# Kernel optimization log

Hardware: AMD Instinct MI355X
Metric: run time of the kernel (lower is better)

## Reference

```python
import jax, jax.numpy as jnp
import numpy as np

N, DIM, HEADS, E = 20000, 256, 4, 100000
C = DIM  # TransformerConv out_channels per head (concat=False averages heads)


def setup_inputs() -> dict:
    key = jax.random.key(0)
    ks = jax.random.split(key, 12)
    s = DIM ** -0.5
    w = lambda k, shape: jax.random.normal(k, shape, jnp.float32) * s
    z = lambda shape: jnp.zeros(shape, jnp.float32)
    return {
        "f_all": jax.random.normal(ks[0], (N, DIM), jnp.float32),
        "edge_index": jax.random.randint(ks[1], (2, E), 0, N),
        "W_gcn": w(ks[2], (DIM, DIM)), "b_gcn": z((DIM,)),
        "W_q": w(ks[3], (DIM, HEADS * C)), "b_q": z((HEADS * C,)),
        "W_k": w(ks[4], (DIM, HEADS * C)), "b_k": z((HEADS * C,)),
        "W_v": w(ks[5], (DIM, HEADS * C)), "b_v": z((HEADS * C,)),
        "W_skip": w(ks[6], (DIM, DIM)), "b_skip": z((DIM,)),
        "W_beta": w(ks[7], (3 * DIM, 1)),
        "W_cnn": w(ks[8], (DIM, DIM)), "b_cnn": z((DIM,)),
    }


def reference(f_all, edge_index, W_gcn, b_gcn, W_q, b_q, W_k, b_k, W_v, b_v,
              W_skip, b_skip, W_beta, W_cnn, b_cnn):
    src, dst = edge_index[0], edge_index[1]

    # --- GCNConv: add self loops, symmetric D^-1/2 (A+I) D^-1/2 normalization ---
    loop = jnp.arange(N)
    s2 = jnp.concatenate([src, loop])
    d2 = jnp.concatenate([dst, loop])
    deg = jax.ops.segment_sum(jnp.ones_like(d2, jnp.float32), d2, N)
    dinv = jnp.where(deg > 0, 1.0 / jnp.sqrt(deg), 0.0)
    norm = dinv[s2] * dinv[d2]                    # [E+N]
    h = f_all @ W_gcn                             # [N, DIM]
    x = jax.ops.segment_sum(h[s2] * norm[:, None], d2, N) + b_gcn
    x = jax.nn.relu(x)

    # --- TransformerConv(heads=H, concat=False, beta=True) ---
    q = (x @ W_q + b_q).reshape(N, HEADS, C)
    k = (x @ W_k + b_k).reshape(N, HEADS, C)
    v = (x @ W_v + b_v).reshape(N, HEADS, C)
    logits = jnp.einsum('ehc,ehc->eh', q[dst], k[src]) / np.float32(np.sqrt(C))
    m = jax.ops.segment_max(logits, dst, N)       # per-target max for stable softmax
    e = jnp.exp(logits - m[dst])
    denom = jax.ops.segment_sum(e, dst, N)
    alpha = e / jnp.maximum(denom[dst], 1e-16)    # [E, H]
    agg = jax.ops.segment_sum(v[src] * alpha[:, :, None], dst, N)  # [N, H, C]
    out = agg.mean(axis=1)                        # concat=False -> head average
    xr = x @ W_skip + b_skip                      # root/skip branch
    beta = jax.nn.sigmoid(jnp.concatenate([out, xr, out - xr], axis=-1) @ W_beta)
    tf = jax.nn.relu(beta * xr + (1.0 - beta) * out)  # [N, DIM]

    # --- Conv1d with kernel (dim,1) on [1,1,dim,N]: per-node linear, output [dim,N] ---
    conv = jnp.einsum('cd,nd->cn', W_cnn, tf) + b_cnn[:, None]  # [DIM, N]
    # torch does .view(1, n_mole, -1) on the [1,dim,1,N] conv output: raw reshape
    return conv.reshape(1, N, DIM)
```

## Files before the change

kernel.cpp:

```cpp
#include <hip/hip_runtime.h>
#include <math.h>

#define DIMC 256
#define NHEAD 4
#define CAP 64

typedef unsigned short bf16u;
typedef __attribute__((ext_vector_type(8))) short bf16x8;
typedef __attribute__((ext_vector_type(4))) float f32x4;

typedef __attribute__((address_space(1))) const unsigned char ga_u8;
typedef __attribute__((address_space(3))) unsigned char lds_u8;
__device__ __forceinline__ void gld_lds16(const void* g, void* l) {
    __builtin_amdgcn_global_load_lds((ga_u8*)g, (lds_u8*)l, 16, 0, 0);
}

__device__ __forceinline__ bf16u f2bf(float f) {
    union { float f; unsigned int i; } c; c.f = f;
    unsigned int r = c.i + 0x7fffu + ((c.i >> 16) & 1u);
    return (bf16u)(r >> 16);
}
__device__ __forceinline__ void store_bf4(bf16u* p, float4 v) {
    ushort4 raw;
    raw.x = f2bf(v.x); raw.y = f2bf(v.y); raw.z = f2bf(v.z); raw.w = f2bf(v.w);
    *(ushort4*)p = raw;
}
__device__ __forceinline__ void load_bf8(const bf16u* p, float* o) {
    bf16x8 raw = *(const bf16x8*)p;
#pragma unroll
    for (int i = 0; i < 8; ++i) {
        union { float f; unsigned int u; } c;
        c.u = ((unsigned int)(unsigned short)raw[i]) << 16;
        o[i] = c.f;
    }
}
__device__ __forceinline__ void store_bf8(bf16u* p, const float* v) {
    bf16x8 raw;
#pragma unroll
    for (int i = 0; i < 8; ++i) raw[i] = (short)f2bf(v[i]);
    *(bf16x8*)p = raw;
}


__global__ void fill_kernel(const int* __restrict__ src, const int* __restrict__ dst,
                            int* __restrict__ cursor, int* __restrict__ srcs, int E) {
    int e = blockIdx.x * 256 + threadIdx.x;
    if (e < E) {
        int d = dst[e];
        int pos = atomicAdd(&cursor[d], 1);
        if (pos < CAP) srcs[d * CAP + pos] = src[e];
    }
}


__global__ __launch_bounds__(256) void prep_kernel(
    const float* __restrict__ f_all, int n4_f,
    const float* __restrict__ W_gcn, const float* __restrict__ W_q,
    const float* __restrict__ W_k, const float* __restrict__ W_v,
    const float* __restrict__ W_skip, const float* __restrict__ W_cnn,
    const float* __restrict__ b_q, const float* __restrict__ b_v,
    const float* __restrict__ b_skip,
    bf16u* __restrict__ xbuf, bf16u* __restrict__ WgcnT,
    bf16u* __restrict__ BTyp, bf16u* __restrict__ BT_vs,
    bf16u* __restrict__ Wcnn_b,
    float* __restrict__ ybias, float* __restrict__ bvm,
    int* __restrict__ cursor, int N) {
    __shared__ __align__(16) char sh[40960];
    int b = blockIdx.x, t = threadIdx.x;
    int nf = (n4_f + 255) >> 8;
    int nz = (N + 255) >> 8;

    if (b < 16) {
        bf16u (*As)[128][32] = (bf16u(*)[128][32])sh;
        bf16u (*Bs)[128][32] = (bf16u(*)[128][32])(sh + 16384);
        bf16u (*Cs)[128]     = (bf16u(*)[128])(sh + 32768);
        int rb = b >> 1, cb = b & 1;
        int h = rb >> 1;
        int j0 = (rb & 1) * 128;
        int t0 = h * 256;
        int w = t >> 6, lane = t & 63;
        int q = lane >> 4, r = lane & 15;
        int wm = (w & 1) * 64, wn = (w >> 1) * 64;
        int srow = t >> 2, scol = (t & 3) * 8;
        const float* ak0 = W_k + (size_t)(j0 + srow) * 1024 + t0 + scol;
        const float* ak1 = W_k + (size_t)(j0 + 64 + srow) * 1024 + t0 + scol;
        const float* bq0 = W_q + (size_t)(cb * 128 + srow) * 1024 + t0 + scol;
        const float* bq1 = W_q + (size_t)(cb * 128 + 64 + srow) * 1024 + t0 + scol;
        auto stage = [&](const float* gp, bf16u* lp) {
            float4 u = *(const float4*)gp, v = *(const float4*)(gp + 4);
            bf16x8 o;
            o[0] = (short)f2bf(u.x); o[1] = (short)f2bf(u.y);
            o[2] = (short)f2bf(u.z); o[3] = (short)f2bf(u.w);
            o[4] = (short)f2bf(v.x); o[5] = (short)f2bf(v.y);
            o[6] = (short)f2bf(v.z); o[7] = (short)f2bf(v.w);
            *(bf16x8*)lp = o;
        };
        f32x4 acc[4][4] = {};
        for (int g = 0; g < 4; ++g) {
            int k0 = g * 64;
            stage(ak0 + k0,      &As[0][srow][scol]);
            stage(ak1 + k0,      &As[0][64 + srow][scol]);
            stage(ak0 + k0 + 32, &As[1][srow][scol]);
            stage(ak1 + k0 + 32, &As[1][64 + srow][scol]);
            stage(bq0 + k0,      &Bs[0][srow][scol]);
            stage(bq1 + k0,      &Bs[0][64 + srow][scol]);
            stage(bq0 + k0 + 32, &Bs[1][srow][scol]);
            stage(bq1 + k0 + 32, &Bs[1][64 + srow][scol]);
            __syncthreads();
#pragma unroll
            for (int ks = 0; ks < 2; ++ks) {
                bf16x8 af[4], bfr[4];
#pragma unroll
                for (int i = 0; i < 4; ++i) af[i] = *(const bf16x8*)&As[ks][wm + i * 16 + r][q * 8];
#pragma unroll
                for (int j = 0; j < 4; ++j) bfr[j] = *(const bf16x8*)&Bs[ks][wn + j * 16 + r][q * 8];
#pragma unroll
                for (int i = 0; i < 4; ++i)
#pragma unroll
                    for (int j = 0; j < 4; ++j)
                        acc[i][j] = __builtin_amdgcn_mfma_f32_16x16x32_bf16(af[i], bfr[j], acc[i][j], 0, 0, 0);
            }
            __syncthreads();
        }
        int bm = rb * 128, bn = cb * 128;
        int rhalf = (w & 1) * 16;
        int colbase = (w >> 1) * 64;
#pragma unroll
        for (int i = 0; i < 4; ++i) {
#pragma unroll
            for (int j = 0; j < 4; ++j)
#pragma unroll
                for (int rg = 0; rg < 4; ++rg)
                    Cs[rhalf + q * 4 + rg][colbase + j * 16 + r] = f2bf(acc[i][j][rg] * 0.0625f);
            __syncthreads();
#pragma unroll
            for (int cpass = 0; cpass < 2; ++cpass) {
                int chunk = cpass * 256 + t;
                int sr = chunk >> 4;
                int c16 = chunk & 15;
                int grow = bm + (sr < 16 ? i * 16 + sr : 64 + i * 16 + (sr - 16));
                *(bf16x8*)&BTyp[(size_t)grow * 256 + bn + c16 * 8] = *(const bf16x8*)&Cs[sr][c16 * 8];
            }
            __syncthreads();
        }
        return;
    }
    b -= 16;
    if (b < nf) {
        int i = b * 256 + t;
        if (i < n4_f) {
            float4 vv = *(const float4*)(f_all + (size_t)i * 4);
            store_bf4(xbuf + (size_t)i * 4, vv);
        }
        return;
    }
    b -= nf;
    if (b < 64) {
        int i = b * 256 + t;
        float4 vv = *(const float4*)(W_cnn + (size_t)i * 4);
        store_bf4(Wcnn_b + (size_t)i * 4, vv);
        return;
    }
    b -= 64;
    if (b < 4) {
        int h = b, j = t;
        const float4* bq4 = (const float4*)(b_q + h * 256);
        const float4* wk4 = (const float4*)(W_k + (size_t)j * 1024 + h * 256);
        float acc = 0.f;
        for (int u = 0; u < 64; ++u) {
            float4 a = bq4[u], w = wk4[u];
            acc += a.x * w.x + a.y * w.y + a.z * w.z + a.w * w.w;
        }
        ybias[h * 256 + j] = acc * 0.0625f;
        return;
    }
    b -= 4;
    if (b < 1) {
        ybias[1024 + t] = b_skip[t];
        bvm[t] = 0.25f * (b_v[t] + b_v[256 + t] + b_v[512 + t] + b_v[768 + t]);
        return;
    }
    b -= 1;
    if (b < nz) {
        int i = b * 256 + t;
        if (i < N) cursor[i] = 0;
        return;
    }
    b -= nz;
    float (*T)[33] = (float(*)[33])sh;
    const float* src; bf16u* dst;
    int inld, inrow0, incol0, outld, outrow0, outcol0;
    if (b < 64) {
        int N0 = (b & 7) * 32, K0 = (b >> 3) * 32;
        src = W_gcn; inld = 256; inrow0 = K0; incol0 = N0;
        dst = WgcnT; outld = 256; outrow0 = N0; outcol0 = K0;
    } else if (b < 128) {
        int bb = b - 64; int N0 = (bb & 7) * 32, K0 = (bb >> 3) * 32;
        src = W_skip; inld = 256; inrow0 = K0; incol0 = N0;
        dst = BTyp;  outld = 256; outrow0 = 1024 + N0; outcol0 = K0;
    } else {
        int bb = b - 128; int jt = bb & 7, ct = (bb >> 3) & 7, hh = bb >> 6;
        src = W_v;  inld = 1024; inrow0 = ct * 32; incol0 = hh * 256 + jt * 32;
        dst = BT_vs; outld = 1024; outrow0 = jt * 32; outcol0 = hh * 256 + ct * 32;
    }
    int tx = t & 31, ty = t >> 5;
#pragma unroll
    for (int i = 0; i < 4; ++i)
        T[ty + 8 * i][tx] = src[(size_t)(inrow0 + ty + 8 * i) * inld + incol0 + tx];
    __syncthreads();
#pragma unroll
    for (int i = 0; i < 4; ++i)
        dst[(size_t)(outrow0 + ty + 8 * i) * outld + outcol0 + tx] = f2bf(T[tx][ty + 8 * i]);
}


template <bool ROWBIAS>
__global__ __launch_bounds__(256) void gemm_tile(const bf16u* __restrict__ A,
                                                 const bf16u* __restrict__ BT,
                                                 const float* __restrict__ bias,
                                                 void* __restrict__ Cout,
                                                 int M, int Nc, int ldc, int K) {
    __shared__ __align__(16) bf16u As[2][128][32];
    __shared__ __align__(16) bf16u Bs[2][128][32];
    int t = threadIdx.x;
    int w = t >> 6, lane = t & 63;
    int q = lane >> 4, r = lane & 15;
    int wm = (w & 1) * 64, wn = (w >> 1) * 64;
    int bm = blockIdx.y * 128, bn = blockIdx.x * 128;

    int srow = t >> 2, scol = (t & 3) * 8;
    int arow0 = bm + srow;      if (arow0 >= M)  arow0 = M - 1;
    int arow1 = bm + 64 + srow; if (arow1 >= M)  arow1 = M - 1;
    int brow0 = bn + srow;      if (brow0 >= Nc) brow0 = Nc - 1;
    int brow1 = bn + 64 + srow; if (brow1 >= Nc) brow1 = Nc - 1;
    const bf16u* a0 = A + (size_t)arow0 * K + scol;
    const bf16u* a1 = A + (size_t)arow1 * K + scol;
    const bf16u* b0 = BT + (size_t)brow0 * K + scol;
    const bf16u* b1 = BT + (size_t)brow1 * K + scol;

    char* As_base = (char*)&As[0][0][0] + w * 1024;
    char* Bs_base = (char*)&Bs[0][0][0] + w * 1024;

    f32x4 acc[4][4] = {};
    int ngroups = K >> 6;
    for (int g = 0; g < ngroups; ++g) {
        int k0 = g * 64;
        gld_lds16(a0 + k0, As_base);
        gld_lds16(a1 + k0, As_base + 4096);
        gld_lds16(b0 + k0, Bs_base);
        gld_lds16(b1 + k0, Bs_base + 4096);
        gld_lds16(a0 + k0 + 32, As_base + 8192);
        gld_lds16(a1 + k0 + 32, As_base + 8192 + 4096);
        gld_lds16(b0 + k0 + 32, Bs_base + 8192);
        gld_lds16(b1 + k0 + 32, Bs_base + 8192 + 4096);
        __syncthreads();
#pragma unroll
        for (int ks = 0; ks < 2; ++ks) {
            bf16x8 af[4], bfr[4];
#pragma unroll
            for (int i = 0; i < 4; ++i) af[i] = *(const bf16x8*)&As[ks][wm + i * 16 + r][q * 8];
#pragma unroll
            for (int j = 0; j < 4; ++j) bfr[j] = *(const bf16x8*)&Bs[ks][wn + j * 16 + r][q * 8];
#pragma unroll
            for (int i = 0; i < 4; ++i)
#pragma unroll
                for (int j = 0; j < 4; ++j)
                    acc[i][j] = __builtin_amdgcn_mfma_f32_16x16x32_bf16(af[i], bfr[j], acc[i][j], 0, 0, 0);
        }
        __syncthreads();
    }

    if (ROWBIAS) {
        float* C = (float*)Cout;
#pragma unroll
        for (int j = 0; j < 4; ++j) {
            int col = bn + wn + j * 16 + r;
            if (col >= Nc) continue;
#pragma unroll
            for (int i = 0; i < 4; ++i)
#pragma unroll
                for (int rg = 0; rg < 4; ++rg) {
                    int row = bm + wm + i * 16 + q * 4 + rg;
                    if (row < M)
                        __builtin_nontemporal_store(acc[i][j][rg] + bias[row],
                                                    &C[(size_t)row * ldc + col]);
                }
        }
    } else {
        __shared__ __align__(16) bf16u Cs[32][128];
        bf16u* C = (bf16u*)Cout;
        float cb4[4];
#pragma unroll
        for (int j = 0; j < 4; ++j) {
            int col = bn + wn + j * 16 + r;
            cb4[j] = bias ? bias[col] : 0.0f;
        }
        int rhalf = (w & 1) * 16;
        int colbase = (w >> 1) * 64;
        __syncthreads();
#pragma unroll
        for (int i = 0; i < 4; ++i) {
#pragma unroll
            for (int j = 0; j < 4; ++j)
#pragma unroll
                for (int rg = 0; rg < 4; ++rg)
                    Cs[rhalf + q * 4 + rg][colbase + j * 16 + r] = f2bf(acc[i][j][rg] + cb4[j]);
            __syncthreads();
#pragma unroll
            for (int cpass = 0; cpass < 2; ++cpass) {
                int chunk = cpass * 256 + t;
                int sr = chunk >> 4;
                int c16 = chunk & 15;
                int grow = bm + (sr < 16 ? i * 16 + sr : 64 + i * 16 + (sr - 16));
                if (grow < M)
                    __builtin_nontemporal_store(*(const bf16x8*)&Cs[sr][c16 * 8],
                                                (bf16x8*)&C[(size_t)grow * ldc + bn + c16 * 8]);
            }
            __syncthreads();
        }
    }
}


__global__ __launch_bounds__(256) void gcn_agg_kernel(const bf16u* __restrict__ h,
                                                      const int* __restrict__ cursor,
                                                      const int* __restrict__ srcs,
                                                      const float* __restrict__ b_gcn,
                                                      bf16u* __restrict__ x, int N) {
    int n = blockIdx.x * 8 + (threadIdx.x >> 5);
    if (n >= N) return;
    int lane = threadIdx.x & 31;
    int cb = lane * 8;
    int cnt = cursor[n]; if (cnt > CAP) cnt = CAP;
    float dn = rsqrtf((float)(cnt + 1));
    float hn[8];
    load_bf8(h + (size_t)n * DIMC + cb, hn);
    int base = n * CAP;
    float acc[8] = {};
    int i = 0;
    for (; i + 4 <= cnt; i += 4) {
        int4 s4 = *(const int4*)(srcs + base + i);
        float d0 = rsqrtf((float)(cursor[s4.x] + 1));
        float d1 = rsqrtf((float)(cursor[s4.y] + 1));
        float d2 = rsqrtf((float)(cursor[s4.z] + 1));
        float d3 = rsqrtf((float)(cursor[s4.w] + 1));
        float h0[8], h1[8], h2[8], h3[8];
        load_bf8(h + (size_t)s4.x * DIMC + cb, h0);
        load_bf8(h + (size_t)s4.y * DIMC + cb, h1);
        load_bf8(h + (size_t)s4.z * DIMC + cb, h2);
        load_bf8(h + (size_t)s4.w * DIMC + cb, h3);
#pragma unroll
        for (int j = 0; j < 8; ++j)
            acc[j] += h0[j] * d0 + h1[j] * d1 + h2[j] * d2 + h3[j] * d3;
    }
    for (; i < cnt; ++i) {
        int s = srcs[base + i];
        float ds = rsqrtf((float)(cursor[s] + 1));
        float hv[8];
        load_bf8(h + (size_t)s * DIMC + cb, hv);
#pragma unroll
        for (int j = 0; j < 8; ++j) acc[j] += hv[j] * ds;
    }
    float4 bg0 = *(const float4*)(b_gcn + cb);
    float4 bg1 = *(const float4*)(b_gcn + cb + 4);
    float bg[8] = {bg0.x, bg0.y, bg0.z, bg0.w, bg1.x, bg1.y, bg1.z, bg1.w};
    float dnn = dn * dn;
    float o[8];
#pragma unroll
    for (int j = 0; j < 8; ++j) o[j] = fmaxf(dn * acc[j] + hn[j] * dnn + bg[j], 0.f);
    store_bf8(x + (size_t)n * DIMC + cb, o);
}


__global__ __launch_bounds__(256) void attn_kernel(const bf16u* __restrict__ Y, int ldy,
                                                   const bf16u* __restrict__ x,
                                                   const int* __restrict__ cursor,
                                                   const int* __restrict__ srcs,
                                                   bf16u* __restrict__ Z, int N) {
    __shared__ __align__(16) bf16u xs[4][2][256];
    int wv = threadIdx.x >> 6;
    int n = blockIdx.x * 4 + wv;
    if (n >= N) return;
    int lane = threadIdx.x & 63;
    int hq = lane >> 4;
    int r = lane & 15;

    float yv[16];
    const bf16u* yrow = Y + (size_t)n * ldy + hq * DIMC + r * 16;
    load_bf8(yrow, yv);
    load_bf8(yrow + 8, yv + 8);

    int cnt = cursor[n]; if (cnt > CAP) cnt = CAP;
    int base = n * CAP;
    float m = -INFINITY, denom = 0.f;
    float acc[16];
#pragma unroll
    for (int j = 0; j < 16; ++j) acc[j] = 0.f;

    int rl = lane >> 5;
    int rc = (lane & 31) * 8;
    bf16u* myslot = &xs[wv][rl][rc];

    int iters = (cnt + 1) >> 1;
    int i0 = 0, i1 = 0;
    if (cnt > 1) {
        int2 ss = *(const int2*)(srcs + base);
        i0 = ss.x; i1 = ss.y;
    } else if (cnt == 1) {
        i0 = srcs[base]; i1 = i0;
    }
    bf16x8 raw;
    if (iters > 0)
        raw = *(const bf16x8*)(x + (size_t)(rl ? i1 : i0) * DIMC + rc);

    for (int it = 0; it < iters; ++it) {
        *(bf16x8*)myslot = raw;
        int e2 = (it + 1) * 2;
        int nv2 = cnt - e2;
        if (nv2 > 1) {
            int2 ss = *(const int2*)(srcs + base + e2);
            i0 = ss.x; i1 = ss.y;
        } else if (nv2 == 1) {
            i0 = srcs[base + e2]; i1 = i0;
        }
        if (nv2 > 0)
            raw = *(const bf16x8*)(x + (size_t)(rl ? i1 : i0) * DIMC + rc);
        asm volatile("s_waitcnt lgkmcnt(0)" ::: "memory");
        float x0[16], x1[16];
        load_bf8(&xs[wv][0][r * 16], x0);
        load_bf8(&xs[wv][0][r * 16 + 8], x0 + 8);
        load_bf8(&xs[wv][1][r * 16], x1);
        load_bf8(&xs[wv][1][r * 16 + 8], x1 + 8);
        float d0 = 0.f, d1 = 0.f;
#pragma unroll
        for (int j = 0; j < 16; ++j) { d0 += yv[j] * x0[j]; d1 += yv[j] * x1[j]; }
#pragma unroll
        for (int msk = 1; msk <= 8; msk <<= 1) {
            d0 += __shfl_xor(d0, msk, 64);
            d1 += __shfl_xor(d1, msk, 64);
        }
        if ((cnt & 1) && it == iters - 1) d1 = -INFINITY;
        float pm = fmaxf(d0, d1);
        if (pm > m + 8.f) {
            float so = __expf(m - pm);
            denom *= so;
#pragma unroll
            for (int j = 0; j < 16; ++j) acc[j] *= so;
            m = pm;
        }
        float p0 = __expf(d0 - m);
        float p1 = __expf(d1 - m);
        denom += p0 + p1;
#pragma unroll
        for (int j = 0; j < 16; ++j) acc[j] += p0 * x0[j] + p1 * x1[j];
        asm volatile("" ::: "memory");
    }

    float inv = 0.25f / fmaxf(denom, 1e-16f);
    float o[16];
#pragma unroll
    for (int j = 0; j < 16; ++j) o[j] = acc[j] * inv;
    bf16u* zrow = Z + (size_t)n * 1024 + hq * DIMC + r * 16;
    store_bf8(zrow, o);
    store_bf8(zrow + 8, o + 8);
}


__global__ __launch_bounds__(256) void beta_kernel(const bf16u* __restrict__ outz,
                                                   const bf16u* __restrict__ Yp, int ldy,
                                                   const float* __restrict__ bvm,
                                                   const float* __restrict__ W_beta,
                                                   const int* __restrict__ cursor,
                                                   bf16u* __restrict__ tf, int N) {
    int n = blockIdx.x * 8 + (threadIdx.x >> 5);
    if (n >= N) return;
    int lane = threadIdx.x & 31;
    int cb = lane * 8;
    float ov[8], xr[8];
    load_bf8(outz + (size_t)n * DIMC + cb, ov);
    load_bf8(Yp + (size_t)n * ldy + 1024 + cb, xr);
    float gate = (cursor[n] > 0) ? 1.f : 0.f;
#pragma unroll
    for (int j = 0; j < 8; ++j) ov[j] += gate * bvm[cb + j];
    float contrib = 0.f;
#pragma unroll
    for (int j = 0; j < 8; ++j) {
        float w1 = W_beta[cb + j];
        float w2 = W_beta[256 + cb + j];
        float w3 = W_beta[512 + cb + j];
        contrib += ov[j] * w1 + xr[j] * w2 + (ov[j] - xr[j]) * w3;
    }
#pragma unroll
    for (int msk = 1; msk <= 16; msk <<= 1) contrib += __shfl_xor(contrib, msk, 64);
    float beta = 1.0f / (1.0f + __expf(-contrib));
    float tv[8];
#pragma unroll
    for (int j = 0; j < 8; ++j) tv[j] = fmaxf(beta * xr[j] + (1.0f - beta) * ov[j], 0.f);
    store_bf8(tf + (size_t)n * DIMC + cb, tv);
}


static inline size_t align_up(size_t x) { return (x + 255) & ~(size_t)255; }

extern "C" void kernel_launch(void* const* d_in, const int* in_sizes, int n_in,
                              void* d_out, int out_size, void* d_ws, size_t ws_size,
                              hipStream_t stream) {
    const float* f_all  = (const float*)d_in[0];
    const int*   eidx   = (const int*)d_in[1];
    const float* W_gcn  = (const float*)d_in[2];
    const float* b_gcn  = (const float*)d_in[3];
    const float* W_q    = (const float*)d_in[4];
    const float* b_q    = (const float*)d_in[5];
    const float* W_k    = (const float*)d_in[6];
    const float* W_v    = (const float*)d_in[8];
    const float* b_v    = (const float*)d_in[9];
    const float* W_skip = (const float*)d_in[10];
    const float* b_skip = (const float*)d_in[11];
    const float* W_beta = (const float*)d_in[12];
    const float* W_cnn  = (const float*)d_in[13];
    const float* b_cnn  = (const float*)d_in[14];

    const int N = in_sizes[0] / DIMC;
    const int E = in_sizes[1] / 2;
    const int* src = eidx;
    const int* dst = eidx + E;

    char* p = (char*)d_ws;
    auto alloc = [&](size_t bytes) { char* r = p; p += align_up(bytes); return r; };
    int*   cursor = (int*)alloc((size_t)N * 4);
    int*   srcs   = (int*)alloc((size_t)N * CAP * 4);
    bf16u* WgcnT  = (bf16u*)alloc(256 * 256 * 2);
    bf16u* BTyp   = (bf16u*)alloc((size_t)1280 * 256 * 2);
    bf16u* BT_vs  = (bf16u*)alloc((size_t)256 * 1024 * 2);
    bf16u* Wcnn_b = (bf16u*)alloc(256 * 256 * 2);
    float* ybias  = (float*)alloc(1280 * 4);
    float* bvm    = (float*)alloc(256 * 4);
    bf16u* xbuf   = (bf16u*)alloc((size_t)N * DIMC * 2);
    bf16u* h      = (bf16u*)alloc((size_t)N * DIMC * 2);
    bf16u* Yp     = (bf16u*)alloc((size_t)N * 1280 * 2);
    bf16u* Z      = (bf16u*)alloc((size_t)N * 1024 * 2);
    bf16u* outz   = (bf16u*)alloc((size_t)N * DIMC * 2);

    int n4_f = N * DIMC / 4;
    int nf = (n4_f + 255) >> 8;
    int nz = (N + 255) >> 8;
    prep_kernel<<<16 + nf + 64 + 4 + 1 + nz + 384, 256, 0, stream>>>(
        f_all, n4_f, W_gcn, W_q, W_k, W_v, W_skip, W_cnn,
        b_q, b_v, b_skip, xbuf, WgcnT, BTyp, BT_vs, Wcnn_b,
        ybias, bvm, cursor, N);

    fill_kernel<<<(E + 255) / 256, 256, 0, stream>>>(src, dst, cursor, srcs, E);

    int mby = (N + 127) / 128;
    gemm_tile<false><<<dim3(2, mby), 256, 0, stream>>>(xbuf, WgcnT, nullptr, h, N, 256, 256, 256);
    gcn_agg_kernel<<<(N + 7) / 8, 256, 0, stream>>>(h, cursor, srcs, b_gcn, xbuf, N);
    gemm_tile<false><<<dim3(10, mby), 256, 0, stream>>>(xbuf, BTyp, ybias, Yp, N, 1280, 1280, 256);
    attn_kernel<<<(N + 3) / 4, 256, 0, stream>>>(Yp, 1280, xbuf, cursor, srcs, Z, N);
    gemm_tile<false><<<dim3(2, mby), 256, 0, stream>>>(Z, BT_vs, nullptr, outz, N, 256, 256, 1024);
    beta_kernel<<<(N + 7) / 8, 256, 0, stream>>>(outz, Yp, 1280, bvm, W_beta, cursor, h, N);
    gemm_tile<true><<<dim3((N + 127) / 128, 2), 256, 0, stream>>>(
        Wcnn_b, h, b_cnn, (float*)d_out, 256, N, N, 256);
}
```

Baseline: 247.0 us.

## Fuse Z-projection GEMM with beta gating into one full-width kernel

Replaces the separate Z×BT_vs GEMM (which wrote outz) and the per-node beta kernel with a single kernel that computes a full 128x256 output tile per block. The epilogue then does the beta dot product, sigmoid gating and ReLU in registers and LDS. This removes the outz intermediate's write and read and one launch. In exchange, the grid drops from 2×mby to mby blocks with larger LDS use and register pressure, which may lower occupancy on a K=1024 GEMM.

Measured after the change: 396.4 us. +60.4%, slower.

```diff
diff --git a/kernel.cpp b/kernel.cpp
--- a/kernel.cpp
+++ b/kernel.cpp
@@ -15,6 +15,9 @@
     __builtin_amdgcn_global_load_lds((ga_u8*)g, (lds_u8*)l, 16, 0, 0);
 }
 
+__device__ __forceinline__ float bf2f(bf16u u) {
+    union { float f; unsigned int i; } c; c.i = ((unsigned int)u) << 16; return c.f;
+}
 __device__ __forceinline__ bf16u f2bf(float f) {
     union { float f; unsigned int i; } c; c.f = f;
     unsigned int r = c.i + 0x7fffu + ((c.i >> 16) & 1u);
@@ -322,6 +325,155 @@
 }
 
 
+__global__ __launch_bounds__(256) void zout_kernel(const bf16u* __restrict__ Z,
+                                                   const bf16u* __restrict__ BT_vs,
+                                                   const bf16u* __restrict__ Yp, int ldy,
+                                                   const float* __restrict__ bvm,
+                                                   const float* __restrict__ W_beta,
+                                                   const int* __restrict__ cursor,
+                                                   bf16u* __restrict__ tf, int M) {
+    __shared__ __align__(16) char sh[53248];
+    bf16u (*As)[128][32] = (bf16u(*)[128][32])sh;
+    bf16u (*Bs)[256][32] = (bf16u(*)[256][32])(sh + 16384);
+    bf16u (*Xr)[256]     = (bf16u(*)[256])sh;
+    bf16u (*Cs)[256]     = (bf16u(*)[256])(sh + 16384);
+    float* gateL = (float*)(sh + 49152);
+    float* w13L  = (float*)(sh + 49664);
+    float* w23L  = (float*)(sh + 50688);
+    float* bvmL  = (float*)(sh + 51712);
+    float* redL  = (float*)(sh + 52736);
+    float* betL  = (float*)(sh + 52992);
+
+    int t = threadIdx.x;
+    int w = t >> 6, lane = t & 63;
+    int q = lane >> 4, r = lane & 15;
+    int wm = (w & 1) * 64, wmIdx = w & 1;
+    int cg = w >> 1;
+    int bm = blockIdx.x * 128;
+
+    {
+        float w1 = W_beta[t], w2 = W_beta[256 + t], w3 = W_beta[512 + t];
+        w13L[t] = w1 + w3;
+        w23L[t] = w2 - w3;
+        bvmL[t] = bvm[t];
+        if (t < 128) {
+            int row = bm + t; if (row >= M) row = M - 1;
+            gateL[t] = (cursor[row] > 0) ? 1.f : 0.f;
+        }
+    }
+
+    int srow = t >> 2, scol = (t & 3) * 8;
+    int arow0 = bm + srow;      if (arow0 >= M) arow0 = M - 1;
+    int arow1 = bm + 64 + srow; if (arow1 >= M) arow1 = M - 1;
+    const bf16u* a0 = Z + (size_t)arow0 * 1024 + scol;
+    const bf16u* a1 = Z + (size_t)arow1 * 1024 + scol;
+    const bf16u* bp[4];
+#pragma unroll
+    for (int h = 0; h < 4; ++h) bp[h] = BT_vs + (size_t)(h * 64 + srow) * 1024 + scol;
+
+    char* As_base = (char*)sh + w * 1024;
+    char* Bs_base = (char*)sh + 16384 + w * 1024;
+
+    f32x4 acc[4][8] = {};
+    for (int g = 0; g < 16; ++g) {
+        int k0 = g * 64;
+        gld_lds16(a0 + k0, As_base);
+        gld_lds16(a1 + k0, As_base + 4096);
+        gld_lds16(a0 + k0 + 32, As_base + 8192);
+        gld_lds16(a1 + k0 + 32, As_base + 8192 + 4096);
+#pragma unroll
+        for (int h = 0; h < 4; ++h) {
+            gld_lds16(bp[h] + k0, Bs_base + h * 4096);
+            gld_lds16(bp[h] + k0 + 32, Bs_base + 16384 + h * 4096);
+        }
+        __syncthreads();
+#pragma unroll
+        for (int ks = 0; ks < 2; ++ks) {
+            bf16x8 af[4], bfr[8];
+#pragma unroll
+            for (int i = 0; i < 4; ++i) af[i] = *(const bf16x8*)&As[ks][wm + i * 16 + r][q * 8];
+#pragma unroll
+            for (int j = 0; j < 8; ++j) {
+                int brow = (j < 4 ? cg * 64 + j * 16 : 128 + cg * 64 + (j - 4) * 16) + r;
+                bfr[j] = *(const bf16x8*)&Bs[ks][brow][q * 8];
+            }
+#pragma unroll
+            for (int i = 0; i < 4; ++i)
+#pragma unroll
+                for (int j = 0; j < 8; ++j)
+                    acc[i][j] = __builtin_amdgcn_mfma_f32_16x16x32_bf16(af[i], bfr[j], acc[i][j], 0, 0, 0);
+        }
+        __syncthreads();
+    }
+
+#pragma unroll 1
+    for (int i = 0; i < 4; ++i) {
+#pragma unroll
+        for (int p = 0; p < 4; ++p) {
+            int idx = p * 256 + t;
+            int rowl = idx >> 5, ch = idx & 31;
+            int grow = bm + (rowl < 16 ? i * 16 + rowl : 64 + i * 16 + (rowl - 16));
+            if (grow >= M) grow = M - 1;
+            gld_lds16(Yp + (size_t)grow * ldy + 1024 + ch * 8,
+                      (char*)sh + p * 4096 + w * 1024);
+        }
+        __syncthreads();
+
+        float contrib[4] = {0.f, 0.f, 0.f, 0.f};
+#pragma unroll
+        for (int j = 0; j < 8; ++j) {
+            int col = (j < 4 ? cg * 64 + j * 16 : 128 + cg * 64 + (j - 4) * 16) + r;
+            float w13c = w13L[col], w23c = w23L[col], bvc = bvmL[col];
+#pragma unroll
+            for (int rg = 0; rg < 4; ++rg) {
+                int rowl32 = wmIdx * 16 + q * 4 + rg;
+                float ov = acc[i][j][rg] + gateL[wm + i * 16 + q * 4 + rg] * bvc;
+                float xr = bf2f(Xr[rowl32][col]);
+                contrib[rg] += ov * w13c + xr * w23c;
+            }
+        }
+#pragma unroll
+        for (int rg = 0; rg < 4; ++rg)
+#pragma unroll
+            for (int msk = 1; msk <= 8; msk <<= 1)
+                contrib[rg] += __shfl_xor(contrib[rg], msk, 64);
+        if (r == 0) {
+#pragma unroll
+            for (int rg = 0; rg < 4; ++rg)
+                redL[cg * 32 + wmIdx * 16 + q * 4 + rg] = contrib[rg];
+        }
+        __syncthreads();
+        if (t < 32) betL[t] = 1.f / (1.f + __expf(-(redL[t] + redL[32 + t])));
+        __syncthreads();
+
+#pragma unroll
+        for (int j = 0; j < 8; ++j) {
+            int col = (j < 4 ? cg * 64 + j * 16 : 128 + cg * 64 + (j - 4) * 16) + r;
+            float bvc = bvmL[col];
+#pragma unroll
+            for (int rg = 0; rg < 4; ++rg) {
+                int rowl32 = wmIdx * 16 + q * 4 + rg;
+                float bet = betL[rowl32];
+                float ov = acc[i][j][rg] + gateL[wm + i * 16 + q * 4 + rg] * bvc;
+                float xr = bf2f(Xr[rowl32][col]);
+                Cs[rowl32][col] = f2bf(fmaxf(bet * xr + (1.f - bet) * ov, 0.f));
+            }
+        }
+        __syncthreads();
+#pragma unroll
+        for (int p = 0; p < 4; ++p) {
+            int idx = p * 256 + t;
+            int sr = idx >> 5, c32 = idx & 31;
+            int grow = bm + (sr < 16 ? i * 16 + sr : 64 + i * 16 + (sr - 16));
+            if (grow < M)
+                __builtin_nontemporal_store(*(const bf16x8*)&Cs[sr][c32 * 8],
+                                            (bf16x8*)&tf[(size_t)grow * 256 + c32 * 8]);
+        }
+        __syncthreads();
+    }
+}
+
+
 __global__ __launch_bounds__(256) void gcn_agg_kernel(const bf16u* __restrict__ h,
                                                       const int* __restrict__ cursor,
                                                       const int* __restrict__ srcs,
@@ -466,40 +618,6 @@
 }
 
 
-__global__ __launch_bounds__(256) void beta_kernel(const bf16u* __restrict__ outz,
-                                                   const bf16u* __restrict__ Yp, int ldy,
-                                                   const float* __restrict__ bvm,
-                                                   const float* __restrict__ W_beta,
-                                                   const int* __restrict__ cursor,
-                                                   bf16u* __restrict__ tf, int N) {
-    int n = blockIdx.x * 8 + (threadIdx.x >> 5);
-    if (n >= N) return;
-    int lane = threadIdx.x & 31;
-    int cb = lane * 8;
-    float ov[8], xr[8];
-    load_bf8(outz + (size_t)n * DIMC + cb, ov);
-    load_bf8(Yp + (size_t)n * ldy + 1024 + cb, xr);
-    float gate = (cursor[n] > 0) ? 1.f : 0.f;
-#pragma unroll
-    for (int j = 0; j < 8; ++j) ov[j] += gate * bvm[cb + j];
-    float contrib = 0.f;
-#pragma unroll
-    for (int j = 0; j < 8; ++j) {
-        float w1 = W_beta[cb + j];
-        float w2 = W_beta[256 + cb + j];
-        float w3 = W_beta[512 + cb + j];
-        contrib += ov[j] * w1 + xr[j] * w2 + (ov[j] - xr[j]) * w3;
-    }
-#pragma unroll
-    for (int msk = 1; msk <= 16; msk <<= 1) contrib += __shfl_xor(contrib, msk, 64);
-    float beta = 1.0f / (1.0f + __expf(-contrib));
-    float tv[8];
-#pragma unroll
-    for (int j = 0; j < 8; ++j) tv[j] = fmaxf(beta * xr[j] + (1.0f - beta) * ov[j], 0.f);
-    store_bf8(tf + (size_t)n * DIMC + cb, tv);
-}
-
-
 static inline size_t align_up(size_t x) { return (x + 255) & ~(size_t)255; }
 
 extern "C" void kernel_launch(void* const* d_in, const int* in_sizes, int n_in,
@@ -539,7 +657,6 @@
     bf16u* h      = (bf16u*)alloc((size_t)N * DIMC * 2);
     bf16u* Yp     = (bf16u*)alloc((size_t)N * 1280 * 2);
     bf16u* Z      = (bf16u*)alloc((size_t)N * 1024 * 2);
-    bf16u* outz   = (bf16u*)alloc((size_t)N * DIMC * 2);
 
     int n4_f = N * DIMC / 4;
     int nf = (n4_f + 255) >> 8;
@@ -556,8 +673,7 @@
     gcn_agg_kernel<<<(N + 7) / 8, 256, 0, stream>>>(h, cursor, srcs, b_gcn, xbuf, N);
     gemm_tile<false><<<dim3(10, mby), 256, 0, stream>>>(xbuf, BTyp, ybias, Yp, N, 1280, 1280, 256);
     attn_kernel<<<(N + 3) / 4, 256, 0, stream>>>(Yp, 1280, xbuf, cursor, srcs, Z, N);
-    gemm_tile<false><<<dim3(2, mby), 256, 0, stream>>>(Z, BT_vs, nullptr, outz, N, 256, 256, 1024);
-    beta_kernel<<<(N + 7) / 8, 256, 0, stream>>>(outz, Yp, 1280, bvm, W_beta, cursor, h, N);
+    zout_kernel<<<mby, 256, 0, stream>>>(Z, BT_vs, Yp, 1280, bvm, W_beta, cursor, h, N);
     gemm_tile<true><<<dim3((N + 127) / 128, 2), 256, 0, stream>>>(
         Wcnn_b, h, b_cnn, (float*)d_out, 256, N, N, 256);
 }
```
